# Kernel optimization log

Hardware: AMD Instinct MI355X
Metric: run time of the kernel (lower is better)

Reference implementation:

```python
import jax, jax.numpy as jnp
import numpy as np

N = 40000   # nodes
E = 640000  # edges (avg degree 16)
D = 128     # feature dim (in_features == out_features)
ALPHA = 0.2 # LeakyReLU negative slope


def setup_inputs() -> dict:
    key = jax.random.key(0)
    ks = jax.random.split(key, 12)
    s = 1.0 / np.sqrt(D)
    return {
        "h":     jax.random.normal(ks[0], (N, D), jnp.float32),
        "src":   jax.random.randint(ks[1], (E,), 0, N, jnp.int32),
        "dst":   jax.random.randint(ks[2], (E,), 0, N, jnp.int32),
        "W":     jax.random.normal(ks[3], (D, D), jnp.float32) * s,
        "b_W":   jnp.zeros((D,), jnp.float32),
        "a_src": jax.random.normal(ks[4], (D,), jnp.float32) * s,
        "a_dst": jax.random.normal(ks[5], (D,), jnp.float32) * s,
        "a_b":   jnp.zeros((1,), jnp.float32),
        "res_W": jax.random.normal(ks[6], (D, D), jnp.float32) * s,
        "res_b": jnp.zeros((D,), jnp.float32),
        "Wi":    jax.random.normal(ks[7], (3 * D, D), jnp.float32) * s,
        "Wh_g":  jax.random.normal(ks[8], (3 * D, D), jnp.float32) * s,
        "bi":    jnp.zeros((3 * D,), jnp.float32),
        "bh":    jnp.zeros((3 * D,), jnp.float32),
    }


def reference(h, src, dst, W, b_W, a_src, a_dst, a_b, res_W, res_b, Wi, Wh_g, bi, bh):
    # --- GAT layer: Wh = W h ---
    Wh = h @ W.T + b_W                                  # [N, D]
    # edge attention: a([Wh_src || Wh_dst]) == Wh_src@a_src + Wh_dst@a_dst + a_b
    s_s = Wh @ a_src                                    # [N]
    s_d = Wh @ a_dst                                    # [N]
    e = jax.nn.leaky_relu(s_s[src] + s_d[dst] + a_b[0], ALPHA)  # [E]
    # segment softmax over incoming edges of each destination node
    m = jax.ops.segment_max(e, dst, num_segments=N)
    m = jnp.where(jnp.isfinite(m), m, 0.0)
    ex = jnp.exp(e - m[dst])                            # [E]
    denom = jax.ops.segment_sum(ex, dst, num_segments=N)
    attn = ex / jnp.where(denom > 0, denom, 1.0)[dst]   # [E]
    # weighted neighbor aggregation (scatter-add on dst)
    h_prime = jax.ops.segment_sum(attn[:, None] * Wh[src], dst, num_segments=N)  # [N, D]
    # residual connection (res=True)
    h_prime = h_prime + h @ res_W.T + res_b
    # --- GRU cell: input = h_prime, hidden = h ---
    gi = h_prime @ Wi.T + bi                            # [N, 3D]
    gh = h @ Wh_g.T + bh                                # [N, 3D]
    i_r, i_z, i_n = jnp.split(gi, 3, axis=-1)
    h_r, h_z, h_n = jnp.split(gh, 3, axis=-1)
    r = jax.nn.sigmoid(i_r + h_r)
    z = jax.nn.sigmoid(i_z + h_z)
    n = jnp.tanh(i_n + r * h_n)
    return (1.0 - z) * n + z * h                        # [N, D]
```

## Files before the change

kernel.cpp:

```cpp
#include <hip/hip_runtime.h>
#include <math.h>

#define NLALPHA 0.2f
#define LOG2E 1.4426950408889634f
#define RT 10

typedef __attribute__((ext_vector_type(8))) short bf16x8;
typedef __attribute__((ext_vector_type(4))) float f32x4;

static __device__ __forceinline__ float fexp(float x) {
    return __builtin_amdgcn_exp2f(x * LOG2E);
}
static __device__ __forceinline__ float fsigmoid(float x) {
    return __builtin_amdgcn_rcpf(1.f + __builtin_amdgcn_exp2f(-LOG2E * x));
}
static __device__ __forceinline__ float ftanh(float x) {
    return 1.f - 2.f * __builtin_amdgcn_rcpf(1.f + __builtin_amdgcn_exp2f(2.f * LOG2E * x));
}
static __device__ __forceinline__ unsigned short f2bf(float f) {
    unsigned int u = __float_as_uint(f);
    return (unsigned short)((u + 0x7fffu + ((u >> 16) & 1u)) >> 16);
}
static __device__ __forceinline__ float bf2f(unsigned short b) {
    return __uint_as_float(((unsigned int)b) << 16);
}

__global__ __launch_bounds__(256) void k_zero(int* __restrict__ hist,
    int* __restrict__ counter, const float* __restrict__ W,
    const float* __restrict__ a_src, const float* __restrict__ a_dst,
    const float* __restrict__ b_W, float* __restrict__ va, float* __restrict__ cc,
    int n, int gZero)
{
    const int b = blockIdx.x;
    if (b < gZero) {
        int i = b * 256 + threadIdx.x;
        if (i < n) hist[i] = 0;
        if (i == 0) counter[0] = 0;
        return;
    }
    const int k = threadIdx.x;
    float cs = 0.f, cd = 0.f;
    if (k < 128) {
        float ss = 0.f, dd = 0.f;
        for (int j = 0; j < 128; ++j) {
            float w = W[j * 128 + k];
            ss = fmaf(w, a_src[j], ss);
            dd = fmaf(w, a_dst[j], dd);
        }
        va[k] = ss;
        va[128 + k] = dd;
        cs = b_W[k] * a_src[k];
        cd = b_W[k] * a_dst[k];
    }
#pragma unroll
    for (int o = 32; o; o >>= 1) { cs += __shfl_down(cs, o); cd += __shfl_down(cd, o); }
    __shared__ float sh[8];
    if ((k & 63) == 0) { sh[(k >> 6) * 2] = cs; sh[(k >> 6) * 2 + 1] = cd; }
    __syncthreads();
    if (k == 0) {
        cc[0] = sh[0] + sh[2] + sh[4] + sh[6];
        cc[1] = sh[1] + sh[3] + sh[5] + sh[7];
    }
}

__global__ __launch_bounds__(256) void k_prep_hist(const float* __restrict__ h,
    const float* __restrict__ W, const float* __restrict__ res_W,
    const float* __restrict__ b_W, const float* __restrict__ res_b,
    const float* __restrict__ Wi, const float* __restrict__ Whg,
    const int* __restrict__ dstv, const float* __restrict__ va,
    const float* __restrict__ cc,
    unsigned short* __restrict__ h_bf, unsigned short* __restrict__ Wcat,
    unsigned short* __restrict__ Wi_bf, unsigned short* __restrict__ Whg_bf,
    float* __restrict__ bias_cat, float* __restrict__ s_s, float* __restrict__ s_d,
    int* __restrict__ hist, int n, int e, int gPrep)
{
    const int b = blockIdx.x;
    if (b < gPrep) {
        int i = b * 256 + threadIdx.x;
        int t = threadIdx.x;
        if (i < n * 16) {
            float4 v0 = ((const float4*)h)[2 * i];
            float4 v1 = ((const float4*)h)[2 * i + 1];
            uint4 o;
            o.x = (unsigned int)f2bf(v0.x) | ((unsigned int)f2bf(v0.y) << 16);
            o.y = (unsigned int)f2bf(v0.z) | ((unsigned int)f2bf(v0.w) << 16);
            o.z = (unsigned int)f2bf(v1.x) | ((unsigned int)f2bf(v1.y) << 16);
            o.w = (unsigned int)f2bf(v1.z) | ((unsigned int)f2bf(v1.w) << 16);
            ((uint4*)h_bf)[i] = o;
            const float* vs = va + (t & 15) * 8;
            const float* vd = vs + 128;
            float ps = v0.x*vs[0] + v0.y*vs[1] + v0.z*vs[2] + v0.w*vs[3]
                     + v1.x*vs[4] + v1.y*vs[5] + v1.z*vs[6] + v1.w*vs[7];
            float pd = v0.x*vd[0] + v0.y*vd[1] + v0.z*vd[2] + v0.w*vd[3]
                     + v1.x*vd[4] + v1.y*vd[5] + v1.z*vd[6] + v1.w*vd[7];
#pragma unroll
            for (int o2 = 1; o2 < 16; o2 <<= 1) {
                ps += __shfl_xor(ps, o2);
                pd += __shfl_xor(pd, o2);
            }
            if ((t & 15) == 0) {
                int row = i >> 4;
                s_s[row] = ps + cc[0];
                s_d[row] = pd + cc[1];
            }
        }
        if (i < 32768) Wcat[i] = f2bf(i < 16384 ? W[i] : res_W[i - 16384]);
        if (i < 49152) { Wi_bf[i] = f2bf(Wi[i]); Whg_bf[i] = f2bf(Whg[i]); }
        if (i < 256) bias_cat[i] = (i < 128) ? b_W[i] : res_b[i - 128];
    } else {
        int i = (b - gPrep) * 256 + threadIdx.x;
        if (i < e) atomicAdd(&hist[dstv[i]], 1);
    }
}

__global__ __launch_bounds__(256) void k_alloc(const int* __restrict__ hist,
    int* __restrict__ counter, int* __restrict__ row_start, int* __restrict__ cursor, int n)
{
    int i = blockIdx.x * 256 + threadIdx.x;
    int lane = threadIdx.x & 63;
    int cnt = (i < n) ? hist[i] : 0;
    int inc = cnt;
#pragma unroll
    for (int o = 1; o < 64; o <<= 1) {
        int v = __shfl_up(inc, o);
        if (lane >= o) inc += v;
    }
    int total = __shfl(inc, 63);
    int base = 0;
    if (lane == 63) base = atomicAdd(counter, total);
    base = __shfl(base, 63);
    int ex = base + inc - cnt;
    if (i < n) { row_start[i] = ex; cursor[i] = ex; }
}

__global__ __launch_bounds__(256, 1) void k_whres_place(
    const unsigned short* __restrict__ h_bf,
    const unsigned short* __restrict__ Wcat, const float* __restrict__ bias_cat,
    unsigned short* __restrict__ Wh, unsigned short* __restrict__ hres,
    const int* __restrict__ dstv, const int* __restrict__ srcv,
    int* __restrict__ cursor, int* __restrict__ esrc,
    int n, int e, int rowBlocks, int gWhres)
{
    const int b = blockIdx.x;
    if (b >= gWhres) {
        int i = (b - gWhres) * 256 + threadIdx.x;
        if (i < e) {
            int p = atomicAdd(&cursor[dstv[i]], 1);
            esrc[p] = srcv[i];
        }
        return;
    }
    const int bx = b % rowBlocks;
    const int by = b / rowBlocks;
    const int t = threadIdx.x;
    const int w = t >> 6, l = t & 63;
    const int lr = l & 15, kq = l >> 4, kg = kq * 8;
    const int jc = by * 64 + w * 16 + lr;
    bf16x8 bw[4];
#pragma unroll
    for (int ks = 0; ks < 4; ++ks)
        bw[ks] = *(const bf16x8*)(Wcat + (size_t)jc * 128 + ks * 32 + kg);
    const float bj = bias_cat[jc];
    unsigned short* dstBase = (jc < 128) ? (Wh + jc) : (hres + (jc - 128));

    int row0 = bx * (16 * RT);
    bf16x8 ac[4];
    {
        const unsigned short* Ap = h_bf + (size_t)min(row0 + lr, n - 1) * 128 + kg;
#pragma unroll
        for (int ks = 0; ks < 4; ++ks) ac[ks] = *(const bf16x8*)(Ap + ks * 32);
    }
    for (int rt = 0; rt < RT && row0 < n; ++rt) {
        const int nrow = row0 + 16;
        bf16x8 an[4];
        if (rt + 1 < RT && nrow < n) {
            const unsigned short* Ap = h_bf + (size_t)min(nrow + lr, n - 1) * 128 + kg;
#pragma unroll
            for (int ks = 0; ks < 4; ++ks) an[ks] = *(const bf16x8*)(Ap + ks * 32);
        }
        f32x4 acc = {};
        acc = __builtin_amdgcn_mfma_f32_16x16x32_bf16(ac[0], bw[0], acc, 0, 0, 0);
        acc = __builtin_amdgcn_mfma_f32_16x16x32_bf16(ac[1], bw[1], acc, 0, 0, 0);
        acc = __builtin_amdgcn_mfma_f32_16x16x32_bf16(ac[2], bw[2], acc, 0, 0, 0);
        acc = __builtin_amdgcn_mfma_f32_16x16x32_bf16(ac[3], bw[3], acc, 0, 0, 0);
#pragma unroll
        for (int r = 0; r < 4; ++r) {
            int row = row0 + kq * 4 + r;
            if (row < n) dstBase[(size_t)row * 128] = f2bf(acc[r] + bj);
        }
#pragma unroll
        for (int ks = 0; ks < 4; ++ks) ac[ks] = an[ks];
        row0 = nrow;
    }
}

__global__ __launch_bounds__(256) void k_attn(const int* __restrict__ row_start,
    const int* __restrict__ hist, const int* __restrict__ esrc,
    const float* __restrict__ s_s, const float* __restrict__ s_d,
    const float* __restrict__ a_b, const unsigned short* __restrict__ Wh,
    const unsigned short* __restrict__ hres, unsigned short* __restrict__ hp, int n)
{
    const int node = (int)((blockIdx.x * 256u + threadIdx.x) >> 6);
    const int l = threadIdx.x & 63;
    if (node >= n) return;
    const int lo = row_start[node];
    const int cnt = hist[node];
    const int hi = lo + cnt;
    const float sdn = s_d[node] + a_b[0];
    const int g = l >> 4;
    const int c = l & 15;

    float sv = 0.f;
    int ssrc = 0;
    float den = 0.f;
    for (int p = lo + l; p < hi; p += 64) {
        int s = esrc[p];
        float ev = s_s[s] + sdn;
        ev = ev > 0.f ? ev : NLALPHA * ev;
        float ex = fexp(ev);
        if (p - lo < 64) { sv = ex; ssrc = s; }
        den += ex;
    }
#pragma unroll
    for (int o = 32; o; o >>= 1) den += __shfl_xor(den, o);
    const float dinv = __builtin_amdgcn_rcpf(den > 0.f ? den : 1.f);

    float acc[8] = {};
    const int q1 = min(cnt, 64);
    for (int q = 0; q < q1; q += 4) {
        int eix = q + g;
        bool valid = eix < cnt;
        int eic = valid ? eix : (cnt - 1);
        float ex = __shfl(sv, eic);
        int s = __shfl(ssrc, eic);
        float wgt = valid ? ex * dinv : 0.f;
        uint4 v = *(const uint4*)(Wh + (size_t)s * 128 + c * 8);
        acc[0] = fmaf(wgt, bf2f((unsigned short)(v.x & 0xffff)), acc[0]);
        acc[1] = fmaf(wgt, bf2f((unsigned short)(v.x >> 16)), acc[1]);
        acc[2] = fmaf(wgt, bf2f((unsigned short)(v.y & 0xffff)), acc[2]);
        acc[3] = fmaf(wgt, bf2f((unsigned short)(v.y >> 16)), acc[3]);
        acc[4] = fmaf(wgt, bf2f((unsigned short)(v.z & 0xffff)), acc[4]);
        acc[5] = fmaf(wgt, bf2f((unsigned short)(v.z >> 16)), acc[5]);
        acc[6] = fmaf(wgt, bf2f((unsigned short)(v.w & 0xffff)), acc[6]);
        acc[7] = fmaf(wgt, bf2f((unsigned short)(v.w >> 16)), acc[7]);
    }
    for (int q = 64; q < cnt; q += 4) {
        int eix = q + g;
        bool valid = eix < cnt;
        int eic = valid ? eix : (cnt - 1);
        int s = esrc[lo + eic];
        float ev = s_s[s] + sdn;
        ev = ev > 0.f ? ev : NLALPHA * ev;
        float wgt = valid ? fexp(ev) * dinv : 0.f;
        uint4 v = *(const uint4*)(Wh + (size_t)s * 128 + c * 8);
        acc[0] = fmaf(wgt, bf2f((unsigned short)(v.x & 0xffff)), acc[0]);
        acc[1] = fmaf(wgt, bf2f((unsigned short)(v.x >> 16)), acc[1]);
        acc[2] = fmaf(wgt, bf2f((unsigned short)(v.y & 0xffff)), acc[2]);
        acc[3] = fmaf(wgt, bf2f((unsigned short)(v.y >> 16)), acc[3]);
        acc[4] = fmaf(wgt, bf2f((unsigned short)(v.z & 0xffff)), acc[4]);
        acc[5] = fmaf(wgt, bf2f((unsigned short)(v.z >> 16)), acc[5]);
        acc[6] = fmaf(wgt, bf2f((unsigned short)(v.w & 0xffff)), acc[6]);
        acc[7] = fmaf(wgt, bf2f((unsigned short)(v.w >> 16)), acc[7]);
    }
#pragma unroll
    for (int k = 0; k < 8; ++k) {
        acc[k] += __shfl_xor(acc[k], 16);
        acc[k] += __shfl_xor(acc[k], 32);
    }
    if (l < 16) {
        uint4 hv = *(const uint4*)(hres + (size_t)node * 128 + l * 8);
        uint4 o;
        o.x = (unsigned int)f2bf(acc[0] + bf2f((unsigned short)(hv.x & 0xffff)))
            | ((unsigned int)f2bf(acc[1] + bf2f((unsigned short)(hv.x >> 16))) << 16);
        o.y = (unsigned int)f2bf(acc[2] + bf2f((unsigned short)(hv.y & 0xffff)))
            | ((unsigned int)f2bf(acc[3] + bf2f((unsigned short)(hv.y >> 16))) << 16);
        o.z = (unsigned int)f2bf(acc[4] + bf2f((unsigned short)(hv.z & 0xffff)))
            | ((unsigned int)f2bf(acc[5] + bf2f((unsigned short)(hv.z >> 16))) << 16);
        o.w = (unsigned int)f2bf(acc[6] + bf2f((unsigned short)(hv.w & 0xffff)))
            | ((unsigned int)f2bf(acc[7] + bf2f((unsigned short)(hv.w >> 16))) << 16);
        *(uint4*)(hp + (size_t)node * 128 + l * 8) = o;
    }
}

__global__ __launch_bounds__(256, 1) void k_gru(const unsigned short* __restrict__ hp_bf,
    const unsigned short* __restrict__ h_bf, const unsigned short* __restrict__ Wi_bf,
    const unsigned short* __restrict__ Whg_bf, const float* __restrict__ bi,
    const float* __restrict__ bh, float* __restrict__ out, int n)
{
    const int t = threadIdx.x;
    const int w = t >> 6, l = t & 63;
    const int lr = l & 15, kq = l >> 4, kg = kq * 8;
    const int c = blockIdx.y * 64 + w * 16 + lr;

    bf16x8 bwi[3][4], bwh[3][4];
#pragma unroll
    for (int g = 0; g < 3; ++g)
#pragma unroll
        for (int ks = 0; ks < 4; ++ks) {
            bwi[g][ks] = *(const bf16x8*)(Wi_bf  + (size_t)(g * 128 + c) * 128 + ks * 32 + kg);
            bwh[g][ks] = *(const bf16x8*)(Whg_bf + (size_t)(g * 128 + c) * 128 + ks * 32 + kg);
        }
    const float biR = bi[c],       bhR = bh[c];
    const float biZ = bi[128 + c], bhZ = bh[128 + c];
    const float biN = bi[256 + c], bhN = bh[256 + c];

    int row0 = blockIdx.x * (16 * RT);
    bf16x8 aPc[4], aHc[4];
    float hvc[4];
    {
        size_t rbase = (size_t)min(row0 + lr, n - 1) * 128 + kg;
#pragma unroll
        for (int ks = 0; ks < 4; ++ks) {
            aPc[ks] = *(const bf16x8*)(hp_bf + rbase + ks * 32);
            aHc[ks] = *(const bf16x8*)(h_bf + rbase + ks * 32);
        }
#pragma unroll
        for (int r = 0; r < 4; ++r)
            hvc[r] = bf2f(h_bf[(size_t)min(row0 + kq * 4 + r, n - 1) * 128 + c]);
    }
    for (int rt = 0; rt < RT && row0 < n; ++rt) {
        const int nrow = row0 + 16;
        bf16x8 aPn[4], aHn[4];
        float hvn[4];
        if (rt + 1 < RT && nrow < n) {
            size_t rbase = (size_t)min(nrow + lr, n - 1) * 128 + kg;
#pragma unroll
            for (int ks = 0; ks < 4; ++ks) {
                aPn[ks] = *(const bf16x8*)(hp_bf + rbase + ks * 32);
                aHn[ks] = *(const bf16x8*)(h_bf + rbase + ks * 32);
            }
#pragma unroll
            for (int r = 0; r < 4; ++r)
                hvn[r] = bf2f(h_bf[(size_t)min(nrow + kq * 4 + r, n - 1) * 128 + c]);
        }

        f32x4 giR = {}, giZ = {}, giN = {}, ghR = {}, ghZ = {}, ghN = {};
#pragma unroll
        for (int ks = 0; ks < 4; ++ks) {
            giR = __builtin_amdgcn_mfma_f32_16x16x32_bf16(aPc[ks], bwi[0][ks], giR, 0, 0, 0);
            ghR = __builtin_amdgcn_mfma_f32_16x16x32_bf16(aHc[ks], bwh[0][ks], ghR, 0, 0, 0);
            giZ = __builtin_amdgcn_mfma_f32_16x16x32_bf16(aPc[ks], bwi[1][ks], giZ, 0, 0, 0);
            ghZ = __builtin_amdgcn_mfma_f32_16x16x32_bf16(aHc[ks], bwh[1][ks], ghZ, 0, 0, 0);
            giN = __builtin_amdgcn_mfma_f32_16x16x32_bf16(aPc[ks], bwi[2][ks], giN, 0, 0, 0);
            ghN = __builtin_amdgcn_mfma_f32_16x16x32_bf16(aHc[ks], bwh[2][ks], ghN, 0, 0, 0);
        }
#pragma unroll
        for (int r = 0; r < 4; ++r) {
            int row = row0 + kq * 4 + r;
            if (row < n) {
                float rg = fsigmoid(giR[r] + biR + ghR[r] + bhR);
                float zg = fsigmoid(giZ[r] + biZ + ghZ[r] + bhZ);
                float ng = ftanh(giN[r] + biN + rg * (ghN[r] + bhN));
                out[(size_t)row * 128 + c] = (1.f - zg) * ng + zg * hvc[r];
            }
        }
#pragma unroll
        for (int ks = 0; ks < 4; ++ks) { aPc[ks] = aPn[ks]; aHc[ks] = aHn[ks]; }
#pragma unroll
        for (int r = 0; r < 4; ++r) hvc[r] = hvn[r];
        row0 = nrow;
    }
}

extern "C" void kernel_launch(void* const* d_in, const int* in_sizes, int n_in,
                              void* d_out, int out_size, void* d_ws, size_t ws_size,
                              hipStream_t stream)
{
    const float* h     = (const float*)d_in[0];
    const int*   srcv  = (const int*)d_in[1];
    const int*   dstv  = (const int*)d_in[2];
    const float* W     = (const float*)d_in[3];
    const float* b_W   = (const float*)d_in[4];
    const float* a_src = (const float*)d_in[5];
    const float* a_dst = (const float*)d_in[6];
    const float* a_b   = (const float*)d_in[7];
    const float* res_W = (const float*)d_in[8];
    const float* res_b = (const float*)d_in[9];
    const float* Wi    = (const float*)d_in[10];
    const float* Whg   = (const float*)d_in[11];
    const float* bi    = (const float*)d_in[12];
    const float* bh    = (const float*)d_in[13];
    float* out = (float*)d_out;
    const int n = in_sizes[0] / 128;
    const int e = in_sizes[1];
    const int rowBlocks = (n + 16 * RT - 1) / (16 * RT);
    const int gZero  = (n + 255) / 256;
    const int gPrep  = (n * 16 + 255) / 256;
    const int gHist  = (e + 255) / 256;
    const int gWhres = rowBlocks * 4;
    const int gPlace = (e + 255) / 256;

    char* p = (char*)d_ws;
    auto carve = [&](size_t bytes) -> char* {
        char* r = p;
        p += (bytes + 255) & ~(size_t)255;
        return r;
    };
    unsigned short* h_bf   = (unsigned short*)carve((size_t)n * 128 * 2);
    unsigned short* Wh     = (unsigned short*)carve((size_t)n * 128 * 2);
    unsigned short* hres   = (unsigned short*)carve((size_t)n * 128 * 2);
    unsigned short* hp_bf  = (unsigned short*)carve((size_t)n * 128 * 2);
    float* s_s             = (float*)carve((size_t)n * 4);
    float* s_d             = (float*)carve((size_t)n * 4);
    int*   hist            = (int*)carve((size_t)n * 4);
    int*   row_start       = (int*)carve((size_t)n * 4);
    int*   cursor          = (int*)carve((size_t)n * 4);
    int*   esrc            = (int*)carve((size_t)e * 4);
    int*   counter         = (int*)carve(4);
    unsigned short* Wcat   = (unsigned short*)carve(32768 * 2);
    unsigned short* Wi_bf  = (unsigned short*)carve(49152 * 2);
    unsigned short* Whg_bf = (unsigned short*)carve(49152 * 2);
    float* bias_cat        = (float*)carve(256 * 4);
    float* va              = (float*)carve(256 * 4);
    float* cc              = (float*)carve(2 * 4);

    k_zero<<<gZero + 1, 256, 0, stream>>>(hist, counter, W, a_src, a_dst, b_W, va, cc, n, gZero);
    k_prep_hist<<<gPrep + gHist, 256, 0, stream>>>(h, W, res_W, b_W, res_b, Wi, Whg, dstv,
                                    va, cc, h_bf, Wcat, Wi_bf, Whg_bf, bias_cat,
                                    s_s, s_d, hist, n, e, gPrep);
    k_alloc<<<(n + 255) / 256, 256, 0, stream>>>(hist, counter, row_start, cursor, n);
    k_whres_place<<<gWhres + gPlace, 256, 0, stream>>>(h_bf, Wcat, bias_cat,
                                    Wh, hres, dstv, srcv, cursor, esrc,
                                    n, e, rowBlocks, gWhres);
    k_attn<<<((size_t)n * 64 + 255) / 256, 256, 0, stream>>>(row_start, hist, esrc, s_s, s_d,
                                                             a_b, Wh, hres, hp_bf, n);
    k_gru<<<dim3(rowBlocks, 2), 256, 0, stream>>>(hp_bf, h_bf, Wi_bf, Whg_bf, bi, bh, out, n);
}
```

Measured before the change: 157.3 us.

## Fuse prefix-sum alloc with Wh/res GEMM and split edge placement into own kernel

Moves the per-node exclusive scan (alloc) into the same launch as the Wh/residual MFMA GEMM blocks, and moves the edge scatter into a separate kernel that runs after it. The launch count stays the same, but the independent GEMM work now overlaps the scan instead of the placement. An empty asm keep-alive pins the weight fragments in registers. The placement pass is no longer overlapped with the GEMM, so the benefit depends on which pairing hides more latency.

```diff
diff --git a/kernel.cpp b/kernel.cpp
--- a/kernel.cpp
+++ b/kernel.cpp
@@ -23,6 +23,10 @@
 }
 static __device__ __forceinline__ float bf2f(unsigned short b) {
     return __uint_as_float(((unsigned int)b) << 16);
+}
+static __device__ __forceinline__ void keep_alive(bf16x8& v) {
+    uint4* q = (uint4*)&v;
+    asm volatile("" : "+v"(q->x), "+v"(q->y), "+v"(q->z), "+v"(q->w));
 }
 
 __global__ __launch_bounds__(256) void k_zero(int* __restrict__ hist,
@@ -113,53 +117,46 @@
     }
 }
 
-__global__ __launch_bounds__(256) void k_alloc(const int* __restrict__ hist,
-    int* __restrict__ counter, int* __restrict__ row_start, int* __restrict__ cursor, int n)
-{
-    int i = blockIdx.x * 256 + threadIdx.x;
-    int lane = threadIdx.x & 63;
-    int cnt = (i < n) ? hist[i] : 0;
-    int inc = cnt;
-#pragma unroll
-    for (int o = 1; o < 64; o <<= 1) {
-        int v = __shfl_up(inc, o);
-        if (lane >= o) inc += v;
-    }
-    int total = __shfl(inc, 63);
-    int base = 0;
-    if (lane == 63) base = atomicAdd(counter, total);
-    base = __shfl(base, 63);
-    int ex = base + inc - cnt;
-    if (i < n) { row_start[i] = ex; cursor[i] = ex; }
-}
-
-__global__ __launch_bounds__(256, 1) void k_whres_place(
+__global__ __launch_bounds__(256, 1) void k_alloc_whres(
+    const int* __restrict__ hist, int* __restrict__ counter,
+    int* __restrict__ row_start, int* __restrict__ cursor,
     const unsigned short* __restrict__ h_bf,
     const unsigned short* __restrict__ Wcat, const float* __restrict__ bias_cat,
     unsigned short* __restrict__ Wh, unsigned short* __restrict__ hres,
-    const int* __restrict__ dstv, const int* __restrict__ srcv,
-    int* __restrict__ cursor, int* __restrict__ esrc,
-    int n, int e, int rowBlocks, int gWhres)
+    int n, int rowBlocks, int gAlloc)
 {
     const int b = blockIdx.x;
-    if (b >= gWhres) {
-        int i = (b - gWhres) * 256 + threadIdx.x;
-        if (i < e) {
-            int p = atomicAdd(&cursor[dstv[i]], 1);
-            esrc[p] = srcv[i];
-        }
+    if (b < gAlloc) {
+        int i = b * 256 + threadIdx.x;
+        int lane = threadIdx.x & 63;
+        int cnt = (i < n) ? hist[i] : 0;
+        int inc = cnt;
+#pragma unroll
+        for (int o = 1; o < 64; o <<= 1) {
+            int v = __shfl_up(inc, o);
+            if (lane >= o) inc += v;
+        }
+        int total = __shfl(inc, 63);
+        int base = 0;
+        if (lane == 63) base = atomicAdd(counter, total);
+        base = __shfl(base, 63);
+        int ex = base + inc - cnt;
+        if (i < n) { row_start[i] = ex; cursor[i] = ex; }
         return;
     }
-    const int bx = b % rowBlocks;
-    const int by = b / rowBlocks;
+    const int bb = b - gAlloc;
+    const int bx = bb % rowBlocks;
+    const int by = bb / rowBlocks;
     const int t = threadIdx.x;
     const int w = t >> 6, l = t & 63;
     const int lr = l & 15, kq = l >> 4, kg = kq * 8;
     const int jc = by * 64 + w * 16 + lr;
     bf16x8 bw[4];
 #pragma unroll
-    for (int ks = 0; ks < 4; ++ks)
+    for (int ks = 0; ks < 4; ++ks) {
         bw[ks] = *(const bf16x8*)(Wcat + (size_t)jc * 128 + ks * 32 + kg);
+        keep_alive(bw[ks]);
+    }
     const float bj = bias_cat[jc];
     unsigned short* dstBase = (jc < 128) ? (Wh + jc) : (hres + (jc - 128));
 
@@ -191,6 +188,16 @@
 #pragma unroll
         for (int ks = 0; ks < 4; ++ks) ac[ks] = an[ks];
         row0 = nrow;
+    }
+}
+
+__global__ void k_place(const int* __restrict__ dstv, const int* __restrict__ srcv,
+    int* cursor, int* esrc, int e)
+{
+    int i = blockIdx.x * 256 + threadIdx.x;
+    if (i < e) {
+        int p = atomicAdd(&cursor[dstv[i]], 1);
+        esrc[p] = srcv[i];
     }
 }
 
@@ -387,8 +394,8 @@
     const int gZero  = (n + 255) / 256;
     const int gPrep  = (n * 16 + 255) / 256;
     const int gHist  = (e + 255) / 256;
+    const int gAlloc = (n + 255) / 256;
     const int gWhres = rowBlocks * 4;
-    const int gPlace = (e + 255) / 256;
 
     char* p = (char*)d_ws;
     auto carve = [&](size_t bytes) -> char* {
@@ -418,10 +425,9 @@
     k_prep_hist<<<gPrep + gHist, 256, 0, stream>>>(h, W, res_W, b_W, res_b, Wi, Whg, dstv,
                                     va, cc, h_bf, Wcat, Wi_bf, Whg_bf, bias_cat,
                                     s_s, s_d, hist, n, e, gPrep);
-    k_alloc<<<(n + 255) / 256, 256, 0, stream>>>(hist, counter, row_start, cursor, n);
-    k_whres_place<<<gWhres + gPlace, 256, 0, stream>>>(h_bf, Wcat, bias_cat,
-                                    Wh, hres, dstv, srcv, cursor, esrc,
-                                    n, e, rowBlocks, gWhres);
+    k_alloc_whres<<<gAlloc + gWhres, 256, 0, stream>>>(hist, counter, row_start, cursor,
+                                    h_bf, Wcat, bias_cat, Wh, hres, n, rowBlocks, gAlloc);
+    k_place<<<(e + 255) / 256, 256, 0, stream>>>(dstv, srcv, cursor, esrc, e);
     k_attn<<<((size_t)n * 64 + 255) / 256, 256, 0, stream>>>(row_start, hist, esrc, s_s, s_d,
                                                              a_b, Wh, hres, hp_bf, n);
     k_gru<<<dim3(rowBlocks, 2), 256, 0, stream>>>(hp_bf, h_bf, Wi_bf, Whg_bf, bi, bh, out, n);
```

Result: slower. 164.2 us (+4.4%).
